# Performance work log

Measured on AMD Instinct MI355X. Metric: run time of the kernel, lower is better.

## Reference

```python
import jax, jax.numpy as jnp
import numpy as np

QUERY_DIM = 1024
CONTEXT_DIM = 768
HEADS = 16
DIM_HEAD = 64
INNER = HEADS * DIM_HEAD  # 1024
SCALE = DIM_HEAD ** -0.5


def setup_inputs() -> dict:
    key = jax.random.key(0)
    ks = jax.random.split(key, 8)
    b, nq, nkv = 4, 2048, 1024
    x = jax.random.normal(ks[0], (b, nq, QUERY_DIM), dtype=jnp.float32)
    context = jax.random.normal(ks[1], (b, nkv, CONTEXT_DIM), dtype=jnp.float32)
    mask = jax.random.randint(ks[2], (b, nkv), 0, 2).astype(jnp.bool_)
    s = 0.02
    Wq = jax.random.normal(ks[3], (QUERY_DIM, INNER), dtype=jnp.float32) * s
    Wk = jax.random.normal(ks[4], (CONTEXT_DIM, INNER), dtype=jnp.float32) * s
    Wv = jax.random.normal(ks[5], (CONTEXT_DIM, INNER), dtype=jnp.float32) * s
    Wo = jax.random.normal(ks[6], (INNER, QUERY_DIM), dtype=jnp.float32) * s
    bo = jnp.zeros((QUERY_DIM,), dtype=jnp.float32)
    return {"x": x, "context": context, "mask": mask,
            "Wq": Wq, "Wk": Wk, "Wv": Wv, "Wo": Wo, "bo": bo}


def reference(x, context, mask, Wq, Wk, Wv, Wo, bo):
    b, nq, _ = x.shape
    nkv = context.shape[1]
    h, d = HEADS, DIM_HEAD
    # QKV projections (no bias, as in nn.Linear(..., bias=False))
    q = (x @ Wq).reshape(b, nq, h, d).transpose(0, 2, 1, 3)       # [b,h,i,d]
    k = (context @ Wk).reshape(b, nkv, h, d).transpose(0, 2, 1, 3)  # [b,h,j,d]
    v = (context @ Wv).reshape(b, nkv, h, d).transpose(0, 2, 1, 3)  # [b,h,j,d]
    sim = jnp.einsum('bhid,bhjd->bhij', q, k) * SCALE
    # mask is per-key [b, j]; broadcast over heads and query positions
    neg = jnp.finfo(sim.dtype).min
    sim = jnp.where(mask[:, None, None, :], sim, neg)
    attn = jax.nn.softmax(sim, axis=-1)
    out = jnp.einsum('bhij,bhjd->bhid', attn, v)                  # [b,h,i,d]
    out = out.transpose(0, 2, 1, 3).reshape(b, nq, h * d)          # [b,i,hd]
    return out @ Wo + bo
```

## Files before the change

### kernel.cpp

```cpp
#include <hip/hip_runtime.h>

typedef unsigned short u16;
typedef __attribute__((ext_vector_type(8))) __bf16 bf16x8;
typedef __attribute__((ext_vector_type(4))) float f32x4;
typedef __attribute__((ext_vector_type(4))) u16 u16x4;

#define NB 4
#define NQ 2048
#define NKV 1024
#define NH 16
#define DH 64
#define DIN 1024
#define DCTX 768
#define NEGBIG -1e30f
#define QSC 0.180336881f

__device__ inline u16 f2bf(float f) {
  unsigned u = __builtin_bit_cast(unsigned, f);
  u += 0x7FFFu + ((u >> 16) & 1u);
  return (u16)(u >> 16);
}

__device__ inline unsigned cvtpk(float lo, float hi) {
  unsigned r;
  asm("v_cvt_pk_bf16_f32 %0, %1, %2" : "=v"(r) : "v"(lo), "v"(hi));
  return r;
}

__device__ inline float exp2a(float x) {
  float r;
  asm("v_exp_f32 %0, %1" : "=v"(r) : "v"(x));
  return r;
}

__global__ __launch_bounds__(256) void build_bias(const void* __restrict__ mask,
                                                  float* __restrict__ biasg) {
  __shared__ int notInt, notFloat;
  if (threadIdx.x == 0) { notInt = 0; notFloat = 0; }
  __syncthreads();
  const unsigned* mw = (const unsigned*)mask;
  int bad_i = 0, bad_f = 0;
#pragma unroll
  for (int e = 0; e < 4; e++) {
    unsigned v = mw[threadIdx.x * 4 + e];
    if (v > 1u) bad_i = 1;
    if (v != 0u && v != 0x3f800000u) bad_f = 1;
  }
  if (bad_i) atomicOr(&notInt, 1);
  if (bad_f) atomicOr(&notFloat, 1);
  __syncthreads();
  const int isInt = !notInt, isFloat = !notFloat;
  for (int i = threadIdx.x; i < NB * NKV; i += 256) {
    bool on;
    if (isInt)        on = ((const int*)mask)[i] != 0;
    else if (isFloat) on = ((const float*)mask)[i] != 0.f;
    else              on = ((const unsigned char*)mask)[i] != 0;
    biasg[i] = on ? 0.f : NEGBIG;
  }
}

__global__ __launch_bounds__(256) void cvt_bf16(const float* __restrict__ in,
                                                u16* __restrict__ out, int n) {
  int i = (blockIdx.x * 256 + threadIdx.x) * 4;
  if (i >= n) return;
  float4 v = *(const float4*)(in + i);
  u16x4 o = { f2bf(v.x), f2bf(v.y), f2bf(v.z), f2bf(v.w) };
  *(u16x4*)(out + i) = o;
}

__global__ __launch_bounds__(256) void transpose_cvt(const float* __restrict__ W,
                                                     u16* __restrict__ Wt, int K, int N) {
  __shared__ float tile[32][33];
  int n0 = blockIdx.x * 32, k0 = blockIdx.y * 32;
  int tx = threadIdx.x & 31, ty = threadIdx.x >> 5;
#pragma unroll
  for (int i = 0; i < 32; i += 8)
    tile[ty + i][tx] = W[(size_t)(k0 + ty + i) * N + n0 + tx];
  __syncthreads();
#pragma unroll
  for (int i = 0; i < 32; i += 8)
    Wt[(size_t)(n0 + ty + i) * K + k0 + tx] = f2bf(tile[tx][ty + i]);
}

__global__ __launch_bounds__(256) void vtrans(const u16* __restrict__ kvb, u16* __restrict__ vtg) {
  __shared__ __align__(16) u16 tile[64][72];
  const int t = threadIdx.x;
  const int jt = blockIdx.x, bh = blockIdx.y;
  const int b = bh >> 4, h = bh & 15;
  const int j0 = jt * 64;
  const int jl = t >> 2, c2 = t & 3;
  const u16* src = kvb + (size_t)(b * 1024 + j0 + jl) * 2048 + 1024 + h * 64 + c2 * 16;
  *(int4*)&tile[jl][c2 * 16]     = *(const int4*)(src);
  *(int4*)&tile[jl][c2 * 16 + 8] = *(const int4*)(src + 8);
  __syncthreads();
  const int dl = t >> 2;
  union { u16 e[16]; int4 q[2]; } pk;
#pragma unroll
  for (int e = 0; e < 16; e++) pk.e[e] = tile[c2 * 16 + e][dl];
  u16* dst = vtg + (size_t)(bh * 64 + dl) * 1024 + j0 + c2 * 16;
  *(int4*)dst       = pk.q[0];
  *(int4*)(dst + 8) = pk.q[1];
}

__global__ __launch_bounds__(256) void gemm_pipe(
    const u16* __restrict__ A0, const u16* __restrict__ B0, void* __restrict__ C0,
    const float* __restrict__ bias0, int N0, int K0, int mode0, int gx0,
    const u16* __restrict__ A1, const u16* __restrict__ B1, void* __restrict__ C1,
    const float* __restrict__ bias1, int N1, int K1, int mode1, int gx1, int split) {
  __shared__ __align__(16) u16 As[3 * 4096];
  __shared__ __align__(16) u16 Bs[3 * 4096];
  const u16 *A, *Bt; void* Cout; const float* bias;
  int N, K, mode, bx, by;
  {
    int bi = blockIdx.x;
    if (bi < split) { A = A0; Bt = B0; Cout = C0; bias = bias0; N = N0; K = K0; mode = mode0; bx = bi % gx0; by = bi / gx0; }
    else { bi -= split; A = A1; Bt = B1; Cout = C1; bias = bias1; N = N1; K = K1; mode = mode1; bx = bi % gx1; by = bi / gx1; }
  }
  const int t = threadIdx.x, w = t >> 6, l = t & 63, g = l >> 4, m16 = l & 15;
  const int brow = by * 128, bcol = bx * 128;
  const int wr = w >> 1, wc = w & 1;
  const int r_a = t >> 2;
  const int kb  = (t & 3) * 8;
  const int nk = K >> 5;
  f32x4 acc[4][4] = {};

#define G_STAGE(ks, bsel)                                                              \
  {                                                                                    \
    int k0_ = (ks) << 5;                                                               \
    _Pragma("unroll")                                                                  \
    for (int i = 0; i < 2; i++) {                                                      \
      const u16* ga = A + (size_t)(brow + i * 64 + r_a) * K + k0_ + kb;                \
      __builtin_amdgcn_global_load_lds(                                                \
          (const __attribute__((address_space(1))) void*)ga,                           \
          (__attribute__((address_space(3))) void*)((char*)As + (bsel) * 8192 + i * 4096 + w * 1024), \
          16, 0, 0);                                                                   \
      const u16* gb = Bt + (size_t)(bcol + i * 64 + r_a) * K + k0_ + kb;               \
      __builtin_amdgcn_global_load_lds(                                                \
          (const __attribute__((address_space(1))) void*)gb,                           \
          (__attribute__((address_space(3))) void*)((char*)Bs + (bsel) * 8192 + i * 4096 + w * 1024), \
          16, 0, 0);                                                                   \
    }                                                                                  \
  }

  G_STAGE(0, 0);
  G_STAGE(1, 1);
  int cur = 0, stg = 2;
  for (int ks = 0; ks < nk; ++ks) {
    if (ks + 1 < nk) asm volatile("s_waitcnt vmcnt(4)" ::: "memory");
    else             asm volatile("s_waitcnt vmcnt(0)" ::: "memory");
    asm volatile("s_barrier" ::: "memory");
    bf16x8 af[4], bfr[4];
#pragma unroll
    for (int m = 0; m < 4; m++)
      af[m] = *(const bf16x8*)(&As[cur * 4096 + (wr * 64 + m * 16 + m16) * 32 + g * 8]);
#pragma unroll
    for (int n = 0; n < 4; n++)
      bfr[n] = *(const bf16x8*)(&Bs[cur * 4096 + (wc * 64 + n * 16 + m16) * 32 + g * 8]);
    if (ks + 2 < nk) G_STAGE(ks + 2, stg);
#pragma unroll
    for (int m = 0; m < 4; m++)
#pragma unroll
      for (int n = 0; n < 4; n++)
        acc[m][n] = __builtin_amdgcn_mfma_f32_16x16x32_bf16(af[m], bfr[n], acc[m][n], 0, 0, 0);
    cur = (cur == 2) ? 0 : cur + 1;
    stg = (stg == 2) ? 0 : stg + 1;
  }
#undef G_STAGE

#pragma unroll
  for (int m = 0; m < 4; m++) {
    int grow = brow + wr * 64 + m * 16 + g * 4;
#pragma unroll
    for (int n = 0; n < 4; n++) {
      int gcol = bcol + wc * 64 + n * 16 + m16;
#pragma unroll
      for (int r = 0; r < 4; r++) {
        size_t off = (size_t)(grow + r) * N + gcol;
        if (mode == 0)      ((float*)Cout)[off] = acc[m][n][r] + bias[gcol];
        else if (mode == 1) ((u16*)Cout)[off] = f2bf(acc[m][n][r]);
        else                ((u16*)Cout)[off] = f2bf(acc[m][n][r] * QSC);
      }
    }
  }
}

__global__ __launch_bounds__(256) void attn(const u16* __restrict__ Q, const u16* __restrict__ Kb,
                                            const u16* __restrict__ Vt_g,
                                            const float* __restrict__ biasg,
                                            u16* __restrict__ O) {
  const int qt = blockIdx.x, h = blockIdx.y, b = blockIdx.z;
  const int t = threadIdx.x, w = t >> 6, l = t & 63, g = l >> 4, m16 = l & 15;
  const int bh = b * NH + h;

  __shared__ __align__(16) u16 Kl[2][4096];
  __shared__ __align__(16) u16 Vt[2][4096];
  __shared__ __align__(16) unsigned Pl[4][16 * 36];
  __shared__ float biasl[NKV];

  for (int i = t; i < NKV; i += 256) biasl[i] = biasg[(size_t)b * NKV + i];

  const int qrow = qt * 64 + w * 16 + m16;
  const u16* qp = Q + (size_t)(b * NQ + qrow) * DIN + h * DH;
  bf16x8 qA0 = *(const bf16x8*)(qp + g * 8);
  bf16x8 qA1 = *(const bf16x8*)(qp + 32 + g * 8);

  f32x4 oA[4] = {};
  float lA = 0.f;

#define STAGE_K(j0, bsel)                                                     \
  {                                                                           \
    _Pragma("unroll")                                                         \
    for (int n = 0; n < 2; n++) {                                             \
      int j_ = n * 32 + (t >> 3);                                             \
      int c_ = (t & 7) ^ (j_ & 7);                                            \
      const u16* gk = Kb + (size_t)(b * NKV + (j0) + j_) * 2048 + h * DH + c_ * 8; \
      __builtin_amdgcn_global_load_lds(                                       \
          (const __attribute__((address_space(1))) void*)gk,                  \
          (__attribute__((address_space(3))) void*)((char*)Kl + (bsel) * 8192 + n * 4096 + t * 16), \
          16, 0, 0);                                                          \
    }                                                                         \
  }
#define STAGE_V(j0, bsel)                                                     \
  {                                                                           \
    _Pragma("unroll")                                                         \
    for (int n = 0; n < 2; n++) {                                             \
      int d_ = n * 32 + (t >> 3);                                             \
      int c_ = (t & 7) ^ (d_ & 7);                                            \
      const u16* gv = Vt_g + (size_t)(bh * 64 + d_) * 1024 + (j0) + c_ * 8;   \
      __builtin_amdgcn_global_load_lds(                                       \
          (const __attribute__((address_space(1))) void*)gv,                  \
          (__attribute__((address_space(3))) void*)((char*)Vt + (bsel) * 8192 + n * 4096 + t * 16), \
          16, 0, 0);                                                          \
    }                                                                         \
  }

  STAGE_K(0, 0);
  STAGE_V(0, 0);
  asm volatile("s_waitcnt vmcnt(0) lgkmcnt(0)" ::: "memory");
  asm volatile("s_barrier" ::: "memory");

  for (int it = 0; it < 16; ++it) {
    const int cur = it & 1, nxt = cur ^ 1;
    const int j0 = it * 64;
    if (it + 1 < 16) {
      STAGE_K(j0 + 64, nxt);
      STAGE_V(j0 + 64, nxt);
    }

    f32x4 sA[4];
#pragma unroll
    for (int jt = 0; jt < 4; jt++) {
      int jr = jt * 16 + m16;
      const u16* krow = &Kl[cur][jr * 64];
      bf16x8 kf0 = *(const bf16x8*)(krow + ((g ^ (jr & 7)) * 8));
      bf16x8 kf1 = *(const bf16x8*)(krow + (((4 + g) ^ (jr & 7)) * 8));
      f32x4 z = {};
      f32x4 t0 = __builtin_amdgcn_mfma_f32_16x16x32_bf16(kf0, qA0, z, 0, 0, 0);
      sA[jt]   = __builtin_amdgcn_mfma_f32_16x16x32_bf16(kf1, qA1, t0, 0, 0, 0);
    }
    float4 b4[4];
#pragma unroll
    for (int jt = 0; jt < 4; jt++) b4[jt] = *(const float4*)&biasl[j0 + jt * 16 + g * 4];

    unsigned* plw = &Pl[w][0];
#pragma unroll
    for (int jt = 0; jt < 4; jt++) {
      float p0 = exp2a(sA[jt][0] + b4[jt].x);
      float p1 = exp2a(sA[jt][1] + b4[jt].y);
      float p2 = exp2a(sA[jt][2] + b4[jt].z);
      float p3 = exp2a(sA[jt][3] + b4[jt].w);
      lA += (p0 + p1) + (p2 + p3);
      uint2 u; u.x = cvtpk(p0, p1); u.y = cvtpk(p2, p3);
      *(uint2*)&plw[m16 * 36 + jt * 8 + 2 * g] = u;
    }
    asm volatile("" ::: "memory");
    bf16x8 pf0 = *(const bf16x8*)&plw[m16 * 36 + 4 * g];
    bf16x8 pf1 = *(const bf16x8*)&plw[m16 * 36 + 16 + 4 * g];
#pragma unroll
    for (int dt = 0; dt < 4; dt++) {
      int d = dt * 16 + m16;
      const u16* vrow = &Vt[cur][d * 64];
      bf16x8 vf0 = *(const bf16x8*)(vrow + ((g ^ (d & 7)) * 8));
      bf16x8 vf1 = *(const bf16x8*)(vrow + (((4 + g) ^ (d & 7)) * 8));
      oA[dt] = __builtin_amdgcn_mfma_f32_16x16x32_bf16(pf0, vf0, oA[dt], 0, 0, 0);
      oA[dt] = __builtin_amdgcn_mfma_f32_16x16x32_bf16(pf1, vf1, oA[dt], 0, 0, 0);
    }
    asm volatile("s_waitcnt vmcnt(0)" ::: "memory");
    asm volatile("s_barrier" ::: "memory");
  }
#undef STAGE_K
#undef STAGE_V

  lA += __shfl_xor(lA, 16); lA += __shfl_xor(lA, 32);
  float invA[4];
#pragma unroll
  for (int r = 0; r < 4; r++) invA[r] = 1.f / __shfl(lA, g * 4 + r);
  u16* op = O + (size_t)(b * NQ + qt * 64 + w * 16) * DIN + h * DH;
#pragma unroll
  for (int dt = 0; dt < 4; dt++)
#pragma unroll
    for (int r = 0; r < 4; r++)
      op[(size_t)(g * 4 + r) * DIN + dt * 16 + m16] = f2bf(oA[dt][r] * invA[r]);
}

extern "C" void kernel_launch(void* const* d_in, const int* in_sizes, int n_in,
                              void* d_out, int out_size, void* d_ws, size_t ws_size,
                              hipStream_t stream) {
  const float* x   = (const float*)d_in[0];
  const float* ctx = (const float*)d_in[1];
  const void*  mask = (const void*)d_in[2];
  const float* Wq  = (const float*)d_in[3];
  const float* Wk  = (const float*)d_in[4];
  const float* Wv  = (const float*)d_in[5];
  const float* Wo  = (const float*)d_in[6];
  const float* bo  = (const float*)d_in[7];
  float* out = (float*)d_out;

  char* ws = (char*)d_ws;
  u16* xb   = (u16*)(ws);
  u16* cb   = (u16*)(ws + 16777216);
  u16* wqt  = (u16*)(ws + 23068672);
  u16* wkv  = (u16*)(ws + 25165824);
  u16* wot  = (u16*)(ws + 28311552);
  u16* qb   = (u16*)(ws + 30408704);
  u16* kvb  = (u16*)(ws + 47185920);
  u16* vtg  = (u16*)(ws + 16777216);
  float* biasg = (float*)(ws + 63963136);
  u16* ab   = xb;

  build_bias<<<1, 256, 0, stream>>>(mask, biasg);
  cvt_bf16<<<8192, 256, 0, stream>>>(x, xb, 8388608);
  cvt_bf16<<<3072, 256, 0, stream>>>(ctx, cb, 3145728);
  transpose_cvt<<<dim3(32, 32), 256, 0, stream>>>(Wq, wqt, 1024, 1024);
  transpose_cvt<<<dim3(32, 24), 256, 0, stream>>>(Wk, wkv, 768, 1024);
  transpose_cvt<<<dim3(32, 24), 256, 0, stream>>>(Wv, wkv + 1024 * 768, 768, 1024);
  transpose_cvt<<<dim3(32, 32), 256, 0, stream>>>(Wo, wot, 1024, 1024);

  gemm_pipe<<<1024, 256, 0, stream>>>(
      xb, wqt, qb, nullptr, 1024, 1024, 2, 8,
      cb, wkv, kvb, nullptr, 2048, 768, 1, 16, 512);

  vtrans<<<dim3(16, 64), 256, 0, stream>>>(kvb, vtg);

  attn<<<dim3(32, 16, 4), 256, 0, stream>>>(qb, kvb, vtg, biasg, ab);

  gemm_pipe<<<512, 256, 0, stream>>>(
      ab, wot, out, bo, 1024, 1024, 0, 8,
      ab, wot, out, bo, 1024, 1024, 0, 8, 512);
}
```

Measured before the change: 290.0 us.

## Use 32x32 MFMA attention with register P shuffle; split GEMM into templated kernels

The attention kernel now has each wave process 32 query rows with 32x32x16 MFMAs. The probability tile is rearranged through cross-lane shuffles instead of an LDS round-trip, and each block covers 128 queries, which halves the grid. The combined QKV GEMM launch is split into two templated gemm_bt launches with a compile-time output mode. The GEMM pipeline also drops from three-stage to two-stage double buffering with a full vmcnt(0) wait every iteration. The aims are fewer LDS round-trips and better MFMA efficiency in attention, at the risk of less latency hiding in the GEMM and lower occupancy in attention.

```diff
diff --git a/kernel.cpp b/kernel.cpp
--- a/kernel.cpp
+++ b/kernel.cpp
@@ -3,6 +3,7 @@
 typedef unsigned short u16;
 typedef __attribute__((ext_vector_type(8))) __bf16 bf16x8;
 typedef __attribute__((ext_vector_type(4))) float f32x4;
+typedef __attribute__((ext_vector_type(16))) float f32x16;
 typedef __attribute__((ext_vector_type(4))) u16 u16x4;
 
 #define NB 4
@@ -102,22 +103,16 @@
   *(int4*)(dst + 8) = pk.q[1];
 }
 
-__global__ __launch_bounds__(256) void gemm_pipe(
-    const u16* __restrict__ A0, const u16* __restrict__ B0, void* __restrict__ C0,
-    const float* __restrict__ bias0, int N0, int K0, int mode0, int gx0,
-    const u16* __restrict__ A1, const u16* __restrict__ B1, void* __restrict__ C1,
-    const float* __restrict__ bias1, int N1, int K1, int mode1, int gx1, int split) {
-  __shared__ __align__(16) u16 As[3 * 4096];
-  __shared__ __align__(16) u16 Bs[3 * 4096];
-  const u16 *A, *Bt; void* Cout; const float* bias;
-  int N, K, mode, bx, by;
-  {
-    int bi = blockIdx.x;
-    if (bi < split) { A = A0; Bt = B0; Cout = C0; bias = bias0; N = N0; K = K0; mode = mode0; bx = bi % gx0; by = bi / gx0; }
-    else { bi -= split; A = A1; Bt = B1; Cout = C1; bias = bias1; N = N1; K = K1; mode = mode1; bx = bi % gx1; by = bi / gx1; }
-  }
+template<int MODE>
+__global__ __launch_bounds__(256) void gemm_bt(const u16* __restrict__ A,
+                                               const u16* __restrict__ Bt,
+                                               void* __restrict__ Cout,
+                                               const float* __restrict__ bias,
+                                               int M, int N, int K) {
+  __shared__ __align__(16) u16 As[2][128 * 32];
+  __shared__ __align__(16) u16 Bs[2][128 * 32];
   const int t = threadIdx.x, w = t >> 6, l = t & 63, g = l >> 4, m16 = l & 15;
-  const int brow = by * 128, bcol = bx * 128;
+  const int brow = blockIdx.y * 128, bcol = blockIdx.x * 128;
   const int wr = w >> 1, wc = w & 1;
   const int r_a = t >> 2;
   const int kb  = (t & 3) * 8;
@@ -143,27 +138,26 @@
   }
 
   G_STAGE(0, 0);
-  G_STAGE(1, 1);
-  int cur = 0, stg = 2;
+  asm volatile("s_waitcnt vmcnt(0)" ::: "memory");
+  __builtin_amdgcn_s_barrier();
+
   for (int ks = 0; ks < nk; ++ks) {
-    if (ks + 1 < nk) asm volatile("s_waitcnt vmcnt(4)" ::: "memory");
-    else             asm volatile("s_waitcnt vmcnt(0)" ::: "memory");
-    asm volatile("s_barrier" ::: "memory");
+    const int cur = ks & 1;
     bf16x8 af[4], bfr[4];
 #pragma unroll
     for (int m = 0; m < 4; m++)
-      af[m] = *(const bf16x8*)(&As[cur * 4096 + (wr * 64 + m * 16 + m16) * 32 + g * 8]);
+      af[m] = *(const bf16x8*)(&As[cur][(wr * 64 + m * 16 + m16) * 32 + g * 8]);
 #pragma unroll
     for (int n = 0; n < 4; n++)
-      bfr[n] = *(const bf16x8*)(&Bs[cur * 4096 + (wc * 64 + n * 16 + m16) * 32 + g * 8]);
-    if (ks + 2 < nk) G_STAGE(ks + 2, stg);
+      bfr[n] = *(const bf16x8*)(&Bs[cur][(wc * 64 + n * 16 + m16) * 32 + g * 8]);
+    if (ks + 1 < nk) G_STAGE(ks + 1, cur ^ 1);
 #pragma unroll
     for (int m = 0; m < 4; m++)
 #pragma unroll
       for (int n = 0; n < 4; n++)
         acc[m][n] = __builtin_amdgcn_mfma_f32_16x16x32_bf16(af[m], bfr[n], acc[m][n], 0, 0, 0);
-    cur = (cur == 2) ? 0 : cur + 1;
-    stg = (stg == 2) ? 0 : stg + 1;
+    asm volatile("s_waitcnt vmcnt(0)" ::: "memory");
+    __builtin_amdgcn_s_barrier();
   }
 #undef G_STAGE
 
@@ -176,8 +170,8 @@
 #pragma unroll
       for (int r = 0; r < 4; r++) {
         size_t off = (size_t)(grow + r) * N + gcol;
-        if (mode == 0)      ((float*)Cout)[off] = acc[m][n][r] + bias[gcol];
-        else if (mode == 1) ((u16*)Cout)[off] = f2bf(acc[m][n][r]);
+        if (MODE == 0)      ((float*)Cout)[off] = acc[m][n][r] + bias[gcol];
+        else if (MODE == 1) ((u16*)Cout)[off] = f2bf(acc[m][n][r]);
         else                ((u16*)Cout)[off] = f2bf(acc[m][n][r] * QSC);
       }
     }
@@ -189,22 +183,23 @@
                                             const float* __restrict__ biasg,
                                             u16* __restrict__ O) {
   const int qt = blockIdx.x, h = blockIdx.y, b = blockIdx.z;
-  const int t = threadIdx.x, w = t >> 6, l = t & 63, g = l >> 4, m16 = l & 15;
+  const int t = threadIdx.x, w = t >> 6, l = t & 63;
+  const int i32 = l & 31, hi = l >> 5;
   const int bh = b * NH + h;
 
   __shared__ __align__(16) u16 Kl[2][4096];
   __shared__ __align__(16) u16 Vt[2][4096];
-  __shared__ __align__(16) unsigned Pl[4][16 * 36];
   __shared__ float biasl[NKV];
 
   for (int i = t; i < NKV; i += 256) biasl[i] = biasg[(size_t)b * NKV + i];
 
-  const int qrow = qt * 64 + w * 16 + m16;
+  const int qrow = qt * 128 + w * 32 + i32;
   const u16* qp = Q + (size_t)(b * NQ + qrow) * DIN + h * DH;
-  bf16x8 qA0 = *(const bf16x8*)(qp + g * 8);
-  bf16x8 qA1 = *(const bf16x8*)(qp + 32 + g * 8);
-
-  f32x4 oA[4] = {};
+  bf16x8 qf[4];
+#pragma unroll
+  for (int c = 0; c < 4; c++) qf[c] = *(const bf16x8*)(qp + c * 16 + hi * 8);
+
+  f32x16 oacc[2] = {};
   float lA = 0.f;
 
 #define STAGE_K(j0, bsel)                                                     \
@@ -236,8 +231,8 @@
 
   STAGE_K(0, 0);
   STAGE_V(0, 0);
-  asm volatile("s_waitcnt vmcnt(0) lgkmcnt(0)" ::: "memory");
-  asm volatile("s_barrier" ::: "memory");
+  asm volatile("s_waitcnt vmcnt(0)" ::: "memory");
+  __builtin_amdgcn_s_barrier();
 
   for (int it = 0; it < 16; ++it) {
     const int cur = it & 1, nxt = cur ^ 1;
@@ -247,60 +242,74 @@
       STAGE_V(j0 + 64, nxt);
     }
 
-    f32x4 sA[4];
-#pragma unroll
-    for (int jt = 0; jt < 4; jt++) {
-      int jr = jt * 16 + m16;
-      const u16* krow = &Kl[cur][jr * 64];
-      bf16x8 kf0 = *(const bf16x8*)(krow + ((g ^ (jr & 7)) * 8));
-      bf16x8 kf1 = *(const bf16x8*)(krow + (((4 + g) ^ (jr & 7)) * 8));
-      f32x4 z = {};
-      f32x4 t0 = __builtin_amdgcn_mfma_f32_16x16x32_bf16(kf0, qA0, z, 0, 0, 0);
-      sA[jt]   = __builtin_amdgcn_mfma_f32_16x16x32_bf16(kf1, qA1, t0, 0, 0, 0);
+    bf16x8 pa[4];
+#pragma unroll
+    for (int jt = 0; jt < 2; jt++) {
+      f32x16 s = {};
+#pragma unroll
+      for (int c = 0; c < 4; c++) {
+        bf16x8 kf = *(const bf16x8*)&Kl[cur][(jt * 32 + i32) * 64 + (((2 * c + hi) ^ (i32 & 7)) * 8)];
+        s = __builtin_amdgcn_mfma_f32_32x32x16_bf16(kf, qf[c], s, 0, 0, 0);
+      }
+      float4 qb4[4];
+#pragma unroll
+      for (int a = 0; a < 4; a++)
+        qb4[a] = *(const float4*)&biasl[j0 + jt * 32 + a * 8 + hi * 4];
+      float p[16];
+#pragma unroll
+      for (int r = 0; r < 16; r++) {
+        const float* bq = (const float*)&qb4[r >> 2];
+        p[r] = exp2a(s[r] + bq[r & 3]);
+      }
+#pragma unroll
+      for (int r = 0; r < 16; r += 4)
+        lA += ((p[r] + p[r + 1]) + (p[r + 2] + p[r + 3]));
+      unsigned u[4][2];
+#pragma unroll
+      for (int a = 0; a < 4; a++) {
+        u[a][0] = cvtpk(p[4 * a], p[4 * a + 1]);
+        u[a][1] = cvtpk(p[4 * a + 2], p[4 * a + 3]);
+      }
+#pragma unroll
+      for (int cc = 0; cc < 2; cc++) {
+        unsigned s0 = hi ? u[2 * cc][0] : u[2 * cc + 1][0];
+        unsigned s1 = hi ? u[2 * cc][1] : u[2 * cc + 1][1];
+        unsigned r0 = __shfl_xor(s0, 32);
+        unsigned r1 = __shfl_xor(s1, 32);
+        union { unsigned uu[4]; bf16x8 v; } pw;
+        pw.uu[0] = hi ? r0 : u[2 * cc][0];
+        pw.uu[1] = hi ? r1 : u[2 * cc][1];
+        pw.uu[2] = hi ? u[2 * cc + 1][0] : r0;
+        pw.uu[3] = hi ? u[2 * cc + 1][1] : r1;
+        pa[jt * 2 + cc] = pw.v;
+      }
     }
-    float4 b4[4];
-#pragma unroll
-    for (int jt = 0; jt < 4; jt++) b4[jt] = *(const float4*)&biasl[j0 + jt * 16 + g * 4];
-
-    unsigned* plw = &Pl[w][0];
-#pragma unroll
-    for (int jt = 0; jt < 4; jt++) {
-      float p0 = exp2a(sA[jt][0] + b4[jt].x);
-      float p1 = exp2a(sA[jt][1] + b4[jt].y);
-      float p2 = exp2a(sA[jt][2] + b4[jt].z);
-      float p3 = exp2a(sA[jt][3] + b4[jt].w);
-      lA += (p0 + p1) + (p2 + p3);
-      uint2 u; u.x = cvtpk(p0, p1); u.y = cvtpk(p2, p3);
-      *(uint2*)&plw[m16 * 36 + jt * 8 + 2 * g] = u;
-    }
-    asm volatile("" ::: "memory");
-    bf16x8 pf0 = *(const bf16x8*)&plw[m16 * 36 + 4 * g];
-    bf16x8 pf1 = *(const bf16x8*)&plw[m16 * 36 + 16 + 4 * g];
-#pragma unroll
-    for (int dt = 0; dt < 4; dt++) {
-      int d = dt * 16 + m16;
-      const u16* vrow = &Vt[cur][d * 64];
-      bf16x8 vf0 = *(const bf16x8*)(vrow + ((g ^ (d & 7)) * 8));
-      bf16x8 vf1 = *(const bf16x8*)(vrow + (((4 + g) ^ (d & 7)) * 8));
-      oA[dt] = __builtin_amdgcn_mfma_f32_16x16x32_bf16(pf0, vf0, oA[dt], 0, 0, 0);
-      oA[dt] = __builtin_amdgcn_mfma_f32_16x16x32_bf16(pf1, vf1, oA[dt], 0, 0, 0);
+#pragma unroll
+    for (int dt = 0; dt < 2; dt++) {
+      const int d = dt * 32 + i32;
+#pragma unroll
+      for (int kc = 0; kc < 4; kc++) {
+        bf16x8 vf = *(const bf16x8*)&Vt[cur][d * 64 + (((2 * kc + hi) ^ (i32 & 7)) * 8)];
+        oacc[dt] = __builtin_amdgcn_mfma_f32_32x32x16_bf16(pa[kc], vf, oacc[dt], 0, 0, 0);
+      }
     }
     asm volatile("s_waitcnt vmcnt(0)" ::: "memory");
-    asm volatile("s_barrier" ::: "memory");
+    __builtin_amdgcn_s_barrier();
   }
 #undef STAGE_K
 #undef STAGE_V
 
-  lA += __shfl_xor(lA, 16); lA += __shfl_xor(lA, 32);
-  float invA[4];
-#pragma unroll
-  for (int r = 0; r < 4; r++) invA[r] = 1.f / __shfl(lA, g * 4 + r);
-  u16* op = O + (size_t)(b * NQ + qt * 64 + w * 16) * DIN + h * DH;
-#pragma unroll
-  for (int dt = 0; dt < 4; dt++)
-#pragma unroll
-    for (int r = 0; r < 4; r++)
-      op[(size_t)(g * 4 + r) * DIN + dt * 16 + m16] = f2bf(oA[dt][r] * invA[r]);
+  lA += __shfl_xor(lA, 32);
+  float inv = 1.f / lA;
+  u16* op = O + (size_t)(b * NQ + qt * 128 + w * 32) * DIN + h * DH;
+#pragma unroll
+  for (int reg = 0; reg < 16; reg++) {
+    const int irow = (reg & 3) + 8 * (reg >> 2) + 4 * hi;
+    const float iv = __shfl(inv, irow);
+#pragma unroll
+    for (int dt = 0; dt < 2; dt++)
+      op[(size_t)irow * DIN + dt * 32 + i32] = f2bf(oacc[dt][reg] * iv);
+  }
 }
 
 extern "C" void kernel_launch(void* const* d_in, const int* in_sizes, int n_in,
@@ -336,15 +345,12 @@
   transpose_cvt<<<dim3(32, 24), 256, 0, stream>>>(Wv, wkv + 1024 * 768, 768, 1024);
   transpose_cvt<<<dim3(32, 32), 256, 0, stream>>>(Wo, wot, 1024, 1024);
 
-  gemm_pipe<<<1024, 256, 0, stream>>>(
-      xb, wqt, qb, nullptr, 1024, 1024, 2, 8,
-      cb, wkv, kvb, nullptr, 2048, 768, 1, 16, 512);
+  gemm_bt<2><<<dim3(8, 64), 256, 0, stream>>>(xb, wqt, qb, nullptr, 8192, 1024, 1024);
+  gemm_bt<1><<<dim3(16, 32), 256, 0, stream>>>(cb, wkv, kvb, nullptr, 4096, 2048, 768);
 
   vtrans<<<dim3(16, 64), 256, 0, stream>>>(kvb, vtg);
 
-  attn<<<dim3(32, 16, 4), 256, 0, stream>>>(qb, kvb, vtg, biasg, ab);
-
-  gemm_pipe<<<512, 256, 0, stream>>>(
-      ab, wot, out, bo, 1024, 1024, 0, 8,
-      ab, wot, out, bo, 1024, 1024, 0, 8, 512);
-}
+  attn<<<dim3(16, 16, 4), 256, 0, stream>>>(qb, kvb, vtg, biasg, ab);
+
+  gemm_bt<0><<<dim3(8, 64), 256, 0, stream>>>(ab, wot, out, bo, 8192, 1024, 1024);
+}
```

Result: faster. 271.0 us (-6.5%).
